# Performance work log

Measured on AMD Instinct MI355X. Metric: run time of the kernel, lower is better.

Reference implementation:

```python
import jax, jax.numpy as jnp
import numpy as np

N_NODES = 100000


def gcn_conv(x, edge_index, edge_weight, W, b):
    """PyG GCNConv: out = D^-1/2 (A + I) D^-1/2 X W + b (self-loop weight 1)."""
    n = x.shape[0]
    src, dst = edge_index[0], edge_index[1]
    loop = jnp.arange(n)
    src_sl = jnp.concatenate([src, loop])
    dst_sl = jnp.concatenate([dst, loop])
    ew_sl = jnp.concatenate([edge_weight, jnp.ones((n,), x.dtype)])
    deg = jax.ops.segment_sum(ew_sl, dst_sl, num_segments=n)  # [N]
    dinv = jnp.where(deg > 0, jax.lax.rsqrt(deg), 0.0)
    norm = dinv[src_sl] * ew_sl * dinv[dst_sl]  # [E+N]
    h = x @ W  # [N, out_dim] dense transform before propagation
    msg = h[src_sl] * norm[:, None]  # gather + scale, [E+N, out_dim]
    out = jax.ops.segment_sum(msg, dst_sl, num_segments=n)  # scatter-add
    return out + b


def setup_inputs() -> dict:
    key = jax.random.key(0)
    ks = jax.random.split(key, 9)
    in_dim, hidden, latent = 128, 64, 32
    n, e = N_NODES, 1600000
    x = jax.random.normal(ks[0], (n, in_dim), dtype=jnp.float32)
    edge_index = jax.random.randint(ks[1], (2, e), 0, n, dtype=jnp.int64)
    edge_weight = jax.random.uniform(ks[2], (e,), dtype=jnp.float32)
    def glorot(k, fan_in, fan_out):
        s = jnp.sqrt(6.0 / (fan_in + fan_out))
        return jax.random.uniform(k, (fan_in, fan_out), jnp.float32, -s, s)
    return {
        "x": x,
        "edge_index": edge_index,
        "edge_weight": edge_weight,
        "W1": glorot(ks[3], in_dim, hidden),
        "b1": jnp.zeros((hidden,), jnp.float32),
        "W_mu": glorot(ks[4], hidden, latent),
        "b_mu": jnp.zeros((latent,), jnp.float32),
        "W_lv": glorot(ks[5], hidden, latent),
        "b_lv": jnp.zeros((latent,), jnp.float32),
    }


def reference(x, edge_index, edge_weight, W1, b1, W_mu, b_mu, W_lv, b_lv):
    h = jax.nn.relu(gcn_conv(x, edge_index, edge_weight, W1, b1))
    mu = gcn_conv(h, edge_index, edge_weight, W_mu, b_mu)
    logvar = gcn_conv(h, edge_index, edge_weight, W_lv, b_lv)
    return (mu, logvar)
```

## Files before the change

kernel.cpp:

```cpp
#include <hip/hip_runtime.h>

static __device__ __forceinline__ float4 ld4(const float* p) { return *(const float4*)p; }
static __device__ __forceinline__ float b2f(unsigned short u) {
    return __uint_as_float((unsigned)u << 16);
}
static __device__ __forceinline__ float b2f_lo(unsigned u) { return __uint_as_float(u << 16); }
static __device__ __forceinline__ float b2f_hi(unsigned u) { return __uint_as_float(u & 0xFFFF0000u); }
static __device__ __forceinline__ unsigned short f2b(float f) {
    unsigned x = __float_as_uint(f);
    return (unsigned short)((x + 0x7FFFu + ((x >> 16) & 1u)) >> 16);
}
static __device__ __forceinline__ unsigned pk2(float lo, float hi) {
    return (unsigned)f2b(lo) | ((unsigned)f2b(hi) << 16);
}

typedef __attribute__((ext_vector_type(8))) short bf16x8;
typedef __attribute__((ext_vector_type(4))) float f32x4;

#define NPB 256
#define CAPE 5120



__global__ __launch_bounds__(256) void k_prep(const float* __restrict__ W1,
                                              const float* __restrict__ Wmu,
                                              const float* __restrict__ Wlv,
                                              unsigned short* __restrict__ Wf1,
                                              unsigned short* __restrict__ Wf2) {
    int tid = threadIdx.x;
    if (blockIdx.x == 0) {
        for (int idx = tid; idx < 2048; idx += 256) {
            int frag = idx >> 6, lane = idx & 63;
            int s = frag & 1, ct = (frag >> 1) & 3, kb = frag >> 3;
            int rA = lane & 15, g8 = (lane >> 4) * 8;
            int c = ct * 16 + rA;
            unsigned short* dstp = Wf1 + frag * 512 + lane * 8;
            for (int j = 0; j < 8; j++) {
                float wv = W1[(size_t)(kb * 32 + g8 + j) * 64 + c];
                unsigned short hi = f2b(wv);
                dstp[j] = (s == 0) ? hi : f2b(wv - b2f(hi));
            }
        }
    } else {
        for (int idx = tid; idx < 1024; idx += 256) {
            int frag = idx >> 6, lane = idx & 63;
            int s = frag & 1, ct = (frag >> 1) & 3, kb = frag >> 3;
            int rA = lane & 15, g8 = (lane >> 4) * 8;
            int c = ct * 16 + rA;
            int k0 = kb * 32 + g8;
            unsigned short* dstp = Wf2 + frag * 512 + lane * 8;
            for (int j = 0; j < 8; j++) {
                float wv = (c < 32) ? Wmu[(size_t)(k0 + j) * 32 + c]
                                    : Wlv[(size_t)(k0 + j) * 32 + (c - 32)];
                unsigned short hi = f2b(wv);
                dstp[j] = (s == 0) ? hi : f2b(wv - b2f(hi));
            }
        }
    }
}

static __device__ __forceinline__ void split8(const float* xv, bf16x8& ah, bf16x8& al) {
    #pragma unroll
    for (int j = 0; j < 8; j++) {
        unsigned u = __float_as_uint(xv[j]);
        float res = xv[j] - __uint_as_float(u & 0xFFFF0000u);
        ah[j] = (short)(u >> 16);
        al[j] = (short)(__float_as_uint(res) >> 16);
    }
}

__global__ __launch_bounds__(256) void k_fused1(const float* __restrict__ A,
                                                const unsigned short* __restrict__ Wf1,
                                                unsigned short* __restrict__ gout,
                                                const int* __restrict__ src,
                                                const int* __restrict__ dst,
                                                const float* __restrict__ ew,
                                                int* __restrict__ bin_cnt,
                                                unsigned long long* __restrict__ ebuf,
                                                int n, int E, int gb, int NB) {
    __shared__ int hist[512];
    __shared__ int hbase[512];
    int tid = threadIdx.x;

    if ((int)blockIdx.x < gb) {
        int row0 = blockIdx.x * 64;
        int w = tid >> 6, lane = tid & 63;
        int rA = lane & 15, g8 = (lane >> 4) * 8;
        int row = row0 + w * 16 + rA;
        const float* xr = A + (size_t)min(row, n - 1) * 128;
        f32x4 acc[4] = {{0.f, 0.f, 0.f, 0.f}, {0.f, 0.f, 0.f, 0.f},
                        {0.f, 0.f, 0.f, 0.f}, {0.f, 0.f, 0.f, 0.f}};
        #pragma unroll
        for (int kb = 0; kb < 4; kb++) {
            float4 v0 = ld4(xr + kb * 32 + g8);
            float4 v1 = ld4(xr + kb * 32 + g8 + 4);
            float xv[8] = {v0.x, v0.y, v0.z, v0.w, v1.x, v1.y, v1.z, v1.w};
            bf16x8 ah, al;
            split8(xv, ah, al);
            const unsigned short* wb = Wf1 + (size_t)(kb * 8) * 512 + lane * 8;
            #pragma unroll
            for (int ct = 0; ct < 4; ct++) {
                bf16x8 bh = *(const bf16x8*)(wb + (ct * 2 + 0) * 512);
                bf16x8 bl = *(const bf16x8*)(wb + (ct * 2 + 1) * 512);
                acc[ct] = __builtin_amdgcn_mfma_f32_16x16x32_bf16(ah, bh, acc[ct], 0, 0, 0);
                acc[ct] = __builtin_amdgcn_mfma_f32_16x16x32_bf16(al, bh, acc[ct], 0, 0, 0);
                acc[ct] = __builtin_amdgcn_mfma_f32_16x16x32_bf16(ah, bl, acc[ct], 0, 0, 0);
            }
        }
        int rbase = row0 + w * 16 + (lane >> 4) * 4;
        #pragma unroll
        for (int reg = 0; reg < 4; reg++) {
            int grow = rbase + reg;
            if (grow < n) {
                #pragma unroll
                for (int ct = 0; ct < 4; ct++)
                    gout[(size_t)grow * 64 + ct * 16 + rA] = f2b(acc[ct][reg]);
            }
        }
    } else {
        for (int j = tid; j < NB; j += 256) hist[j] = 0;
        __syncthreads();
        int e0 = ((int)blockIdx.x - gb) * 4096;
        unsigned long long pk[16]; int bb[16]; int loc[16];
        #pragma unroll
        for (int j = 0; j < 16; j++) {
            int e = e0 + j * 256 + tid;
            if (e < E) {
                int s = src[e];
                int d = dst[e];
                float w = ew[e];
                bb[j] = d >> 8;
                pk[j] = ((unsigned long long)__float_as_uint(w) << 32) |
                        (unsigned)((d & (NPB - 1)) << 17) | (unsigned)s;
                loc[j] = atomicAdd(&hist[bb[j]], 1);
            } else bb[j] = -1;
        }
        __syncthreads();
        for (int j = tid; j < NB; j += 256) hbase[j] = atomicAdd(&bin_cnt[j], hist[j]);
        __syncthreads();
        #pragma unroll
        for (int j = 0; j < 16; j++) {
            if (bb[j] >= 0)
                ebuf[(size_t)bb[j] * CAPE + hbase[bb[j]] + loc[j]] = pk[j];
        }
    }
}

__global__ __launch_bounds__(512) void k_csr_build(const unsigned long long* __restrict__ ebuf,
                                                   const int* __restrict__ bin_cnt,
                                                   int2* __restrict__ rowcnt,
                                                   float* __restrict__ dinv,
                                                   unsigned long long* __restrict__ csr,
                                                   unsigned short* __restrict__ h0,
                                                   int n) {
    __shared__ unsigned long long eL[CAPE];
    __shared__ unsigned cntL[NPB];
    __shared__ unsigned ewsL[NPB];
    __shared__ unsigned fillL[NPB];
    __shared__ int scanL[512];
    __shared__ int rowL[NPB];
    __shared__ float dinvL[NPB];
    __shared__ int binbase_s;
    int b = blockIdx.x;
    int tid = threadIdx.x;
    if (tid < NPB) { cntL[tid] = 0; ewsL[tid] = 0; fillL[tid] = 0; }
    scanL[tid] = (tid < b) ? bin_cnt[tid] : 0;
    __syncthreads();
    int m = bin_cnt[b];
    const unsigned long long* eb = ebuf + (size_t)b * CAPE;
    for (int i = tid; i < m; i += 512) {
        unsigned long long pk = eb[i];
        eL[i] = pk;
        int ld = (int)((pk >> 17) & (NPB - 1));
        float w = __uint_as_float((unsigned)(pk >> 32));
        atomicAdd(&cntL[ld], 1u);
        atomicAdd(&ewsL[ld], (unsigned)(w * 16777216.0f));
    }
    __syncthreads();
    #pragma unroll
    for (int off = 256; off > 0; off >>= 1) {
        if (tid < off) scanL[tid] += scanL[tid + off];
        __syncthreads();
    }
    if (tid == 0) binbase_s = scanL[0];
    __syncthreads();
    int v = (tid < NPB) ? (int)cntL[tid] : 0;
    scanL[tid] = v;
    __syncthreads();
    #pragma unroll
    for (int off = 1; off < 512; off <<= 1) {
        int t = (tid >= off) ? scanL[tid - off] : 0;
        __syncthreads();
        scanL[tid] += t;
        __syncthreads();
    }
    if (tid < NPB) {
        int rp = binbase_s + scanL[tid] - v;
        rowL[tid] = rp;
        float dv = rsqrtf(1.0f + (float)ewsL[tid] * (1.0f / 16777216.0f));
        dinvL[tid] = dv;
        int node = b * NPB + tid;
        if (node < n) {
            rowcnt[node] = make_int2(rp, v);
            dinv[node] = dv;
        }
    }
    __syncthreads();
    for (int i = tid; i < m; i += 512) {
        unsigned long long pk = eL[i];
        int s = (int)(pk & 0x1FFFF);
        int ld = (int)((pk >> 17) & (NPB - 1));
        int pos = rowL[ld] + (int)atomicAdd(&fillL[ld], 1u);
        csr[pos] = (unsigned long long)(unsigned)s | (pk & 0xFFFFFFFF00000000ull);
    }
    for (int idx = tid; idx < NPB * 8; idx += 512) {
        int ln = idx >> 3;
        int node = b * NPB + ln;
        if (node < n) {
            float sc = dinvL[ln];
            unsigned short* hp = h0 + (size_t)node * 64 + (idx & 7) * 8;
            uint4 u = *(uint4*)hp;
            u.x = pk2(b2f_lo(u.x) * sc, b2f_hi(u.x) * sc);
            u.y = pk2(b2f_lo(u.y) * sc, b2f_hi(u.y) * sc);
            u.z = pk2(b2f_lo(u.z) * sc, b2f_hi(u.z) * sc);
            u.w = pk2(b2f_lo(u.w) * sc, b2f_hi(u.w) * sc);
            *(uint4*)hp = u;
        }
    }
}

__global__ __launch_bounds__(256) void k_gemm2(const unsigned short* __restrict__ h,
                                               const unsigned short* __restrict__ Wf2,
                                               const float* __restrict__ dinv,
                                               unsigned short* __restrict__ out, int n) {
    int tid = threadIdx.x;
    int row0 = blockIdx.x * 64;
    int w = tid >> 6, lane = tid & 63;
    int rA = lane & 15, g8 = (lane >> 4) * 8;
    int row = row0 + w * 16 + rA;
    const unsigned short* hr = h + (size_t)min(row, n - 1) * 64;
    f32x4 acc[4] = {{0.f, 0.f, 0.f, 0.f}, {0.f, 0.f, 0.f, 0.f},
                    {0.f, 0.f, 0.f, 0.f}, {0.f, 0.f, 0.f, 0.f}};
    #pragma unroll
    for (int kb = 0; kb < 2; kb++) {
        bf16x8 a = *(const bf16x8*)(hr + kb * 32 + g8);
        const unsigned short* wb = Wf2 + (size_t)(kb * 8) * 512 + lane * 8;
        #pragma unroll
        for (int ct = 0; ct < 4; ct++) {
            bf16x8 bh = *(const bf16x8*)(wb + (ct * 2 + 0) * 512);
            bf16x8 bl = *(const bf16x8*)(wb + (ct * 2 + 1) * 512);
            acc[ct] = __builtin_amdgcn_mfma_f32_16x16x32_bf16(a, bh, acc[ct], 0, 0, 0);
            acc[ct] = __builtin_amdgcn_mfma_f32_16x16x32_bf16(a, bl, acc[ct], 0, 0, 0);
        }
    }
    int rbase = row0 + w * 16 + (lane >> 4) * 4;
    #pragma unroll
    for (int reg = 0; reg < 4; reg++) {
        int grow = rbase + reg;
        if (grow < n) {
            float sc = dinv[grow];
            #pragma unroll
            for (int ct = 0; ct < 4; ct++)
                out[(size_t)grow * 64 + ct * 16 + rA] = f2b(acc[ct][reg] * sc);
        }
    }
}

static __device__ __forceinline__ void acc8(float* a, uint4 r, float wt) {
    a[0] = fmaf(b2f_lo(r.x), wt, a[0]); a[1] = fmaf(b2f_hi(r.x), wt, a[1]);
    a[2] = fmaf(b2f_lo(r.y), wt, a[2]); a[3] = fmaf(b2f_hi(r.y), wt, a[3]);
    a[4] = fmaf(b2f_lo(r.z), wt, a[4]); a[5] = fmaf(b2f_hi(r.z), wt, a[5]);
    a[6] = fmaf(b2f_lo(r.w), wt, a[6]); a[7] = fmaf(b2f_hi(r.w), wt, a[7]);
}

template<bool RELU, bool SPLIT_OUT>
__global__ __launch_bounds__(256) void k_prop(const unsigned short* __restrict__ g,
                                              const int2* __restrict__ csr,
                                              const int2* __restrict__ rowcnt,
                                              const float* __restrict__ dinv,
                                              const float* __restrict__ bias0,
                                              const float* __restrict__ bias1,
                                              void* __restrict__ outv, int n) {
    int node = blockIdx.x * 4 + (threadIdx.x >> 6);
    if (node >= n) return;
    int lane = threadIdx.x & 63;
    int q = lane >> 3;
    int t = lane & 7;
    uint4 sr = *(const uint4*)(g + (size_t)node * 64 + t * 8);
    int2 rc = rowcnt[node];
    const int2* ep = csr + rc.x;
    int m = rc.y;
    float a[8] = {};
    for (int e = 0; e < m; e += 32) {
        int e1 = e + q, e2 = e1 + 8, e3 = e1 + 16, e4 = e1 + 24;
        int i1 = min(e1, m - 1), i2 = min(e2, m - 1);
        int i3 = min(e3, m - 1), i4 = min(e4, m - 1);
        int2 p1 = ep[i1];
        int2 p2 = ep[i2];
        int2 p3 = ep[i3];
        int2 p4 = ep[i4];
        uint4 r1 = *(const uint4*)(g + (size_t)p1.x * 64 + t * 8);
        uint4 r2 = *(const uint4*)(g + (size_t)p2.x * 64 + t * 8);
        uint4 r3 = *(const uint4*)(g + (size_t)p3.x * 64 + t * 8);
        uint4 r4 = *(const uint4*)(g + (size_t)p4.x * 64 + t * 8);
        float w1 = (e1 < m) ? __int_as_float(p1.y) : 0.f;
        float w2 = (e2 < m) ? __int_as_float(p2.y) : 0.f;
        float w3 = (e3 < m) ? __int_as_float(p3.y) : 0.f;
        float w4 = (e4 < m) ? __int_as_float(p4.y) : 0.f;
        acc8(a, r1, w1);
        acc8(a, r2, w2);
        acc8(a, r3, w3);
        acc8(a, r4, w4);
    }
    #pragma unroll
    for (int i = 0; i < 8; i++) {
        a[i] += __shfl_xor(a[i], 8);
        a[i] += __shfl_xor(a[i], 16);
        a[i] += __shfl_xor(a[i], 32);
    }
    if (q != 0) return;
    a[0] += b2f_lo(sr.x); a[1] += b2f_hi(sr.x);
    a[2] += b2f_lo(sr.y); a[3] += b2f_hi(sr.y);
    a[4] += b2f_lo(sr.z); a[5] += b2f_hi(sr.z);
    a[6] += b2f_lo(sr.w); a[7] += b2f_hi(sr.w);
    float di = dinv[node];
    #pragma unroll
    for (int i = 0; i < 8; i++) a[i] *= di;
    if (!SPLIT_OUT) {
        float4 b0 = ld4(bias0 + t * 8);
        float4 b1 = ld4(bias0 + t * 8 + 4);
        a[0] += b0.x; a[1] += b0.y; a[2] += b0.z; a[3] += b0.w;
        a[4] += b1.x; a[5] += b1.y; a[6] += b1.z; a[7] += b1.w;
        if (RELU) {
            #pragma unroll
            for (int i = 0; i < 8; i++) a[i] = fmaxf(a[i], 0.f);
        }
        uint4 u = make_uint4(pk2(a[0], a[1]), pk2(a[2], a[3]),
                             pk2(a[4], a[5]), pk2(a[6], a[7]));
        *(uint4*)((unsigned short*)outv + (size_t)node * 64 + t * 8) = u;
    } else {
        float* out = (float*)outv;
        const float* bp = (t < 4) ? (bias0 + t * 8) : (bias1 + (t - 4) * 8);
        size_t base = (t < 4) ? ((size_t)node * 32 + t * 8)
                              : ((size_t)n * 32 + (size_t)node * 32 + (t - 4) * 8);
        float4 b0 = ld4(bp);
        float4 b1 = ld4(bp + 4);
        float4 v0 = make_float4(a[0] + b0.x, a[1] + b0.y, a[2] + b0.z, a[3] + b0.w);
        float4 v1 = make_float4(a[4] + b1.x, a[5] + b1.y, a[6] + b1.z, a[7] + b1.w);
        *(float4*)&out[base] = v0;
        *(float4*)&out[base + 4] = v1;
    }
}

extern "C" void kernel_launch(void* const* d_in, const int* in_sizes, int n_in,
                              void* d_out, int out_size, void* d_ws, size_t ws_size,
                              hipStream_t stream) {
    const float* x   = (const float*)d_in[0];
    const int*   ei  = (const int*)d_in[1];
    const float* ew  = (const float*)d_in[2];
    const float* W1  = (const float*)d_in[3];
    const float* b1  = (const float*)d_in[4];
    const float* Wmu = (const float*)d_in[5];
    const float* bmu = (const float*)d_in[6];
    const float* Wlv = (const float*)d_in[7];
    const float* blv = (const float*)d_in[8];
    float* outp = (float*)d_out;

    const int n = in_sizes[0] / 128;
    const int E = in_sizes[2];
    const int* src = ei;
    const int* dst = ei + E;
    const int NB = (n + NPB - 1) / NPB;

    size_t o = 0;
    auto alloc = [&](size_t bytes) { void* p = (char*)d_ws + o; o += (bytes + 511) & ~(size_t)511; return p; };
    int*   bin_cnt  = (int*)alloc((size_t)NB * 4);
    int2*  rowcnt   = (int2*)alloc((size_t)n * 8);
    float* dinv     = (float*)alloc((size_t)n * 4);
    unsigned long long* csr  = (unsigned long long*)alloc((size_t)E * 8);
    unsigned long long* ebuf = (unsigned long long*)alloc((size_t)NB * CAPE * 8);
    unsigned short* g0 = (unsigned short*)alloc((size_t)n * 64 * 2);
    unsigned short* h  = (unsigned short*)alloc((size_t)n * 64 * 2);
    unsigned short* Wf1 = (unsigned short*)alloc(32 * 512 * 2);
    unsigned short* Wf2 = (unsigned short*)alloc(16 * 512 * 2);
    unsigned short* g2 = g0;

    const int gb = (n + 63) / 64;
    const int bb = (E + 4095) / 4096;

    k_prep<<<2, 256, 0, stream>>>(W1, Wmu, Wlv, Wf1, Wf2);
    hipMemsetAsync(bin_cnt, 0, (size_t)NB * 4, stream);
    k_fused1<<<gb + bb, 256, 0, stream>>>(x, Wf1, g0, src, dst, ew,
                                          bin_cnt, ebuf, n, E, gb, NB);
    k_csr_build<<<NB, 512, 0, stream>>>(ebuf, bin_cnt, rowcnt, dinv, csr, g0, n);
    k_prop<true, false><<<(n + 3) / 4, 256, 0, stream>>>(g0, (const int2*)csr, rowcnt, dinv,
                                                         b1, nullptr, h, n);
    k_gemm2<<<gb, 256, 0, stream>>>(h, Wf2, dinv, g2, n);
    k_prop<false, true><<<(n + 3) / 4, 256, 0, stream>>>(g2, (const int2*)csr, rowcnt, dinv,
                                                         bmu, blv, outp, n);
}
```

Before: 278.3 us.

## Split CSR build into count and scatter kernels, apply source dinv in propagation

Replaces the single per-bin CSR build kernel (prefix scan over all bins, shared-memory edge staging, in-place rescaling of g0) with two kernels. A count kernel takes each bin's base from an atomic counter and computes row offsets and dinv. A two-blocks-per-bin scatter kernel then places edges through global atomic fill counters. The first propagation now multiplies each edge weight by dinv of its source on the fly instead of pre-scaling h0. It also adds a fast path for rows with at most 16 edges, and moves the bin_cnt memset into the prep kernel. This gives the CSR build more parallelism and drops the g0 rewrite pass, but adds an extra dinv gather per edge and a launch, and edge order within a CSR row becomes nondeterministic.

```diff
diff --git a/kernel.cpp b/kernel.cpp
--- a/kernel.cpp
+++ b/kernel.cpp
@@ -26,7 +26,9 @@
                                               const float* __restrict__ Wmu,
                                               const float* __restrict__ Wlv,
                                               unsigned short* __restrict__ Wf1,
-                                              unsigned short* __restrict__ Wf2) {
+                                              unsigned short* __restrict__ Wf2,
+                                              int* __restrict__ bin_cnt,
+                                              int* __restrict__ ctr, int NB) {
     int tid = threadIdx.x;
     if (blockIdx.x == 0) {
         for (int idx = tid; idx < 2048; idx += 256) {
@@ -41,7 +43,7 @@
                 dstp[j] = (s == 0) ? hi : f2b(wv - b2f(hi));
             }
         }
-    } else {
+    } else if (blockIdx.x == 1) {
         for (int idx = tid; idx < 1024; idx += 256) {
             int frag = idx >> 6, lane = idx & 63;
             int s = frag & 1, ct = (frag >> 1) & 3, kb = frag >> 3;
@@ -56,6 +58,9 @@
                 dstp[j] = (s == 0) ? hi : f2b(wv - b2f(hi));
             }
         }
+    } else {
+        for (int j = tid; j < NB; j += 256) bin_cnt[j] = 0;
+        if (tid == 0) *ctr = 0;
     }
 }
 
@@ -81,15 +86,15 @@
     __shared__ int hist[512];
     __shared__ int hbase[512];
     int tid = threadIdx.x;
-
-    if ((int)blockIdx.x < gb) {
-        int row0 = blockIdx.x * 64;
+    int bid = blockIdx.x;
+
+    if (bid < gb) {
+        int row0 = bid * 64;
         int w = tid >> 6, lane = tid & 63;
         int rA = lane & 15, g8 = (lane >> 4) * 8;
         int row = row0 + w * 16 + rA;
         const float* xr = A + (size_t)min(row, n - 1) * 128;
-        f32x4 acc[4] = {{0.f, 0.f, 0.f, 0.f}, {0.f, 0.f, 0.f, 0.f},
-                        {0.f, 0.f, 0.f, 0.f}, {0.f, 0.f, 0.f, 0.f}};
+        f32x4 acc[4] = {{0.f,0.f,0.f,0.f},{0.f,0.f,0.f,0.f},{0.f,0.f,0.f,0.f},{0.f,0.f,0.f,0.f}};
         #pragma unroll
         for (int kb = 0; kb < 4; kb++) {
             float4 v0 = ld4(xr + kb * 32 + g8);
@@ -120,7 +125,7 @@
     } else {
         for (int j = tid; j < NB; j += 256) hist[j] = 0;
         __syncthreads();
-        int e0 = ((int)blockIdx.x - gb) * 4096;
+        int e0 = (bid - gb) * 4096;
         unsigned long long pk[16]; int bb[16]; int loc[16];
         #pragma unroll
         for (int j = 0; j < 16; j++) {
@@ -146,86 +151,66 @@
     }
 }
 
-__global__ __launch_bounds__(512) void k_csr_build(const unsigned long long* __restrict__ ebuf,
-                                                   const int* __restrict__ bin_cnt,
-                                                   int2* __restrict__ rowcnt,
-                                                   float* __restrict__ dinv,
-                                                   unsigned long long* __restrict__ csr,
-                                                   unsigned short* __restrict__ h0,
-                                                   int n) {
-    __shared__ unsigned long long eL[CAPE];
+__global__ __launch_bounds__(256) void k_count(const unsigned long long* __restrict__ ebuf,
+                                               const int* __restrict__ bin_cnt,
+                                               int* __restrict__ ctr,
+                                               int2* __restrict__ rowcnt,
+                                               float* __restrict__ dinv,
+                                               int* __restrict__ fillg,
+                                               int n) {
     __shared__ unsigned cntL[NPB];
     __shared__ unsigned ewsL[NPB];
-    __shared__ unsigned fillL[NPB];
-    __shared__ int scanL[512];
-    __shared__ int rowL[NPB];
-    __shared__ float dinvL[NPB];
+    __shared__ int scanL[NPB];
     __shared__ int binbase_s;
     int b = blockIdx.x;
     int tid = threadIdx.x;
-    if (tid < NPB) { cntL[tid] = 0; ewsL[tid] = 0; fillL[tid] = 0; }
-    scanL[tid] = (tid < b) ? bin_cnt[tid] : 0;
+    cntL[tid] = 0; ewsL[tid] = 0;
     __syncthreads();
     int m = bin_cnt[b];
+    if (tid == 0) binbase_s = atomicAdd(ctr, m);
     const unsigned long long* eb = ebuf + (size_t)b * CAPE;
-    for (int i = tid; i < m; i += 512) {
+    for (int i = tid; i < m; i += 256) {
         unsigned long long pk = eb[i];
-        eL[i] = pk;
         int ld = (int)((pk >> 17) & (NPB - 1));
         float w = __uint_as_float((unsigned)(pk >> 32));
         atomicAdd(&cntL[ld], 1u);
         atomicAdd(&ewsL[ld], (unsigned)(w * 16777216.0f));
     }
     __syncthreads();
-    #pragma unroll
-    for (int off = 256; off > 0; off >>= 1) {
-        if (tid < off) scanL[tid] += scanL[tid + off];
-        __syncthreads();
-    }
-    if (tid == 0) binbase_s = scanL[0];
-    __syncthreads();
-    int v = (tid < NPB) ? (int)cntL[tid] : 0;
+    int v = (int)cntL[tid];
     scanL[tid] = v;
     __syncthreads();
     #pragma unroll
-    for (int off = 1; off < 512; off <<= 1) {
+    for (int off = 1; off < NPB; off <<= 1) {
         int t = (tid >= off) ? scanL[tid - off] : 0;
         __syncthreads();
         scanL[tid] += t;
         __syncthreads();
     }
-    if (tid < NPB) {
+    int node = b * NPB + tid;
+    if (node < n) {
         int rp = binbase_s + scanL[tid] - v;
-        rowL[tid] = rp;
-        float dv = rsqrtf(1.0f + (float)ewsL[tid] * (1.0f / 16777216.0f));
-        dinvL[tid] = dv;
-        int node = b * NPB + tid;
-        if (node < n) {
-            rowcnt[node] = make_int2(rp, v);
-            dinv[node] = dv;
-        }
-    }
-    __syncthreads();
-    for (int i = tid; i < m; i += 512) {
-        unsigned long long pk = eL[i];
+        rowcnt[node] = make_int2(rp, v);
+        fillg[node] = rp;
+        dinv[node] = rsqrtf(1.0f + (float)ewsL[tid] * (1.0f / 16777216.0f));
+    }
+}
+
+__global__ __launch_bounds__(256) void k_scatter2(const unsigned long long* __restrict__ ebuf,
+                                                  const int* __restrict__ bin_cnt,
+                                                  int* __restrict__ fillg,
+                                                  int2* __restrict__ csr, int nb) {
+    int b = blockIdx.x >> 1;
+    int half = blockIdx.x & 1;
+    int m = bin_cnt[b];
+    const unsigned long long* eb = ebuf + (size_t)b * CAPE;
+    int nbase = b * NPB;
+    for (int i = half * 256 + threadIdx.x; i < m; i += 512) {
+        unsigned long long pk = eb[i];
         int s = (int)(pk & 0x1FFFF);
         int ld = (int)((pk >> 17) & (NPB - 1));
-        int pos = rowL[ld] + (int)atomicAdd(&fillL[ld], 1u);
-        csr[pos] = (unsigned long long)(unsigned)s | (pk & 0xFFFFFFFF00000000ull);
-    }
-    for (int idx = tid; idx < NPB * 8; idx += 512) {
-        int ln = idx >> 3;
-        int node = b * NPB + ln;
-        if (node < n) {
-            float sc = dinvL[ln];
-            unsigned short* hp = h0 + (size_t)node * 64 + (idx & 7) * 8;
-            uint4 u = *(uint4*)hp;
-            u.x = pk2(b2f_lo(u.x) * sc, b2f_hi(u.x) * sc);
-            u.y = pk2(b2f_lo(u.y) * sc, b2f_hi(u.y) * sc);
-            u.z = pk2(b2f_lo(u.z) * sc, b2f_hi(u.z) * sc);
-            u.w = pk2(b2f_lo(u.w) * sc, b2f_hi(u.w) * sc);
-            *(uint4*)hp = u;
-        }
+        int pos = atomicAdd(&fillg[nbase + ld], 1);
+        csr[pos] = make_int2(s, (int)(pk >> 32));
     }
 }
 
@@ -239,8 +224,7 @@
     int rA = lane & 15, g8 = (lane >> 4) * 8;
     int row = row0 + w * 16 + rA;
     const unsigned short* hr = h + (size_t)min(row, n - 1) * 64;
-    f32x4 acc[4] = {{0.f, 0.f, 0.f, 0.f}, {0.f, 0.f, 0.f, 0.f},
-                    {0.f, 0.f, 0.f, 0.f}, {0.f, 0.f, 0.f, 0.f}};
+    f32x4 acc[4] = {{0.f,0.f,0.f,0.f},{0.f,0.f,0.f,0.f},{0.f,0.f,0.f,0.f},{0.f,0.f,0.f,0.f}};
     #pragma unroll
     for (int kb = 0; kb < 2; kb++) {
         bf16x8 a = *(const bf16x8*)(hr + kb * 32 + g8);
@@ -273,7 +257,7 @@
     a[6] = fmaf(b2f_lo(r.w), wt, a[6]); a[7] = fmaf(b2f_hi(r.w), wt, a[7]);
 }
 
-template<bool RELU, bool SPLIT_OUT>
+template<bool RELU, bool SPLIT_OUT, bool DSCALE>
 __global__ __launch_bounds__(256) void k_prop(const unsigned short* __restrict__ g,
                                               const int2* __restrict__ csr,
                                               const int2* __restrict__ rowcnt,
@@ -291,26 +275,44 @@
     const int2* ep = csr + rc.x;
     int m = rc.y;
     float a[8] = {};
-    for (int e = 0; e < m; e += 32) {
-        int e1 = e + q, e2 = e1 + 8, e3 = e1 + 16, e4 = e1 + 24;
+    if (m > 0 && m <= 16) {
+        int e1 = q, e2 = q + 8;
         int i1 = min(e1, m - 1), i2 = min(e2, m - 1);
-        int i3 = min(e3, m - 1), i4 = min(e4, m - 1);
         int2 p1 = ep[i1];
         int2 p2 = ep[i2];
-        int2 p3 = ep[i3];
-        int2 p4 = ep[i4];
         uint4 r1 = *(const uint4*)(g + (size_t)p1.x * 64 + t * 8);
         uint4 r2 = *(const uint4*)(g + (size_t)p2.x * 64 + t * 8);
-        uint4 r3 = *(const uint4*)(g + (size_t)p3.x * 64 + t * 8);
-        uint4 r4 = *(const uint4*)(g + (size_t)p4.x * 64 + t * 8);
         float w1 = (e1 < m) ? __int_as_float(p1.y) : 0.f;
         float w2 = (e2 < m) ? __int_as_float(p2.y) : 0.f;
-        float w3 = (e3 < m) ? __int_as_float(p3.y) : 0.f;
-        float w4 = (e4 < m) ? __int_as_float(p4.y) : 0.f;
+        if (DSCALE) { w1 *= dinv[p1.x]; w2 *= dinv[p2.x]; }
         acc8(a, r1, w1);
         acc8(a, r2, w2);
-        acc8(a, r3, w3);
-        acc8(a, r4, w4);
+    } else {
+        for (int e = 0; e < m; e += 32) {
+            int e1 = e + q, e2 = e1 + 8, e3 = e1 + 16, e4 = e1 + 24;
+            int i1 = min(e1, m - 1), i2 = min(e2, m - 1);
+            int i3 = min(e3, m - 1), i4 = min(e4, m - 1);
+            int2 p1 = ep[i1];
+            int2 p2 = ep[i2];
+            int2 p3 = ep[i3];
+            int2 p4 = ep[i4];
+            uint4 r1 = *(const uint4*)(g + (size_t)p1.x * 64 + t * 8);
+            uint4 r2 = *(const uint4*)(g + (size_t)p2.x * 64 + t * 8);
+            uint4 r3 = *(const uint4*)(g + (size_t)p3.x * 64 + t * 8);
+            uint4 r4 = *(const uint4*)(g + (size_t)p4.x * 64 + t * 8);
+            float w1 = (e1 < m) ? __int_as_float(p1.y) : 0.f;
+            float w2 = (e2 < m) ? __int_as_float(p2.y) : 0.f;
+            float w3 = (e3 < m) ? __int_as_float(p3.y) : 0.f;
+            float w4 = (e4 < m) ? __int_as_float(p4.y) : 0.f;
+            if (DSCALE) {
+                w1 *= dinv[p1.x]; w2 *= dinv[p2.x];
+                w3 *= dinv[p3.x]; w4 *= dinv[p4.x];
+            }
+            acc8(a, r1, w1);
+            acc8(a, r2, w2);
+            acc8(a, r3, w3);
+            acc8(a, r4, w4);
+        }
     }
     #pragma unroll
     for (int i = 0; i < 8; i++) {
@@ -319,11 +321,12 @@
         a[i] += __shfl_xor(a[i], 32);
     }
     if (q != 0) return;
-    a[0] += b2f_lo(sr.x); a[1] += b2f_hi(sr.x);
-    a[2] += b2f_lo(sr.y); a[3] += b2f_hi(sr.y);
-    a[4] += b2f_lo(sr.z); a[5] += b2f_hi(sr.z);
-    a[6] += b2f_lo(sr.w); a[7] += b2f_hi(sr.w);
     float di = dinv[node];
+    float ss = DSCALE ? di : 1.f;
+    a[0] += ss * b2f_lo(sr.x); a[1] += ss * b2f_hi(sr.x);
+    a[2] += ss * b2f_lo(sr.y); a[3] += ss * b2f_hi(sr.y);
+    a[4] += ss * b2f_lo(sr.z); a[5] += ss * b2f_hi(sr.z);
+    a[6] += ss * b2f_lo(sr.w); a[7] += ss * b2f_hi(sr.w);
     #pragma unroll
     for (int i = 0; i < 8; i++) a[i] *= di;
     if (!SPLIT_OUT) {
@@ -375,9 +378,11 @@
     size_t o = 0;
     auto alloc = [&](size_t bytes) { void* p = (char*)d_ws + o; o += (bytes + 511) & ~(size_t)511; return p; };
     int*   bin_cnt  = (int*)alloc((size_t)NB * 4);
+    int*   ctr      = (int*)alloc(512);
     int2*  rowcnt   = (int2*)alloc((size_t)n * 8);
     float* dinv     = (float*)alloc((size_t)n * 4);
-    unsigned long long* csr  = (unsigned long long*)alloc((size_t)E * 8);
+    int*   fillg    = (int*)alloc((size_t)n * 4);
+    int2*  csr      = (int2*)alloc((size_t)E * 8);
     unsigned long long* ebuf = (unsigned long long*)alloc((size_t)NB * CAPE * 8);
     unsigned short* g0 = (unsigned short*)alloc((size_t)n * 64 * 2);
     unsigned short* h  = (unsigned short*)alloc((size_t)n * 64 * 2);
@@ -388,14 +393,14 @@
     const int gb = (n + 63) / 64;
     const int bb = (E + 4095) / 4096;
 
-    k_prep<<<2, 256, 0, stream>>>(W1, Wmu, Wlv, Wf1, Wf2);
-    hipMemsetAsync(bin_cnt, 0, (size_t)NB * 4, stream);
+    k_prep<<<3, 256, 0, stream>>>(W1, Wmu, Wlv, Wf1, Wf2, bin_cnt, ctr, NB);
     k_fused1<<<gb + bb, 256, 0, stream>>>(x, Wf1, g0, src, dst, ew,
                                           bin_cnt, ebuf, n, E, gb, NB);
-    k_csr_build<<<NB, 512, 0, stream>>>(ebuf, bin_cnt, rowcnt, dinv, csr, g0, n);
-    k_prop<true, false><<<(n + 3) / 4, 256, 0, stream>>>(g0, (const int2*)csr, rowcnt, dinv,
-                                                         b1, nullptr, h, n);
+    k_count<<<NB, 256, 0, stream>>>(ebuf, bin_cnt, ctr, rowcnt, dinv, fillg, n);
+    k_scatter2<<<NB * 2, 256, 0, stream>>>(ebuf, bin_cnt, fillg, csr, NB);
+    k_prop<true, false, true><<<(n + 3) / 4, 256, 0, stream>>>(g0, csr, rowcnt, dinv,
+                                                               b1, nullptr, h, n);
     k_gemm2<<<gb, 256, 0, stream>>>(h, Wf2, dinv, g2, n);
-    k_prop<false, true><<<(n + 3) / 4, 256, 0, stream>>>(g2, (const int2*)csr, rowcnt, dinv,
-                                                         bmu, blv, outp, n);
-}
+    k_prop<false, true, false><<<(n + 3) / 4, 256, 0, stream>>>(g2, csr, rowcnt, dinv,
+                                                                bmu, blv, outp, n);
+}
```

Measured after the change: 302.3 us. +8.7%, slower.
